# Kernel tuning notes

Measured on AMD Instinct MI355X. Metric: run time of the kernel, lower is better.

## Reference

```python
import jax, jax.numpy as jnp
import numpy as np

NUM_LAYERS = 6
KS = 5  # kernel_size; also attention window size K
EPS_IN = 1e-5  # torch InstanceNorm1d default eps


def _conv1d(x, w, b, d, p):
    # x: [N,C,L], w: [O,I,KS], dilated 'same' conv
    y = jax.lax.conv_general_dilated(x, w, window_strides=(1,), padding=[(p, p)],
                                     rhs_dilation=(d,), dimension_numbers=('NCH', 'OIH', 'NCH'))
    return y + b[None, :, None]


def _pw(x, w, b):
    # pointwise (1x1) conv: x [N,C,L], w [O,C]
    return jnp.einsum('oc,ncl->nol', w, x) + b[None, :, None]


def _layer(x, x_cross, pr, d):
    C, L = x.shape[1], x.shape[2]
    p = (KS // 2) * d  # padding
    conv_w, conv_b, qw, qb, kw, kb, vw, vb, f1w, f1b, f2w, f2b = pr
    out1 = _conv1d(x, conv_w, conv_b, d, p)
    xc = jnp.concatenate([x, x_cross], axis=1)
    q = _pw(xc, qw, qb)            # [N,C,L]
    k = _pw(xc, kw, kb)
    v = _pw(x, vw, vb)
    kp = jnp.pad(k, ((0, 0), (0, 0), (p, p)))
    vp = jnp.pad(v, ((0, 0), (0, 0), (p, p)))
    # attn index for query q, slot j is (q + j*d) into padded axis -> shifted slices
    win_k = jnp.stack([kp[:, :, j * d:j * d + L] for j in range(KS)], axis=-1)  # [N,C,L,K]
    win_v = jnp.stack([vp[:, :, j * d:j * d + L] for j in range(KS)], axis=-1)
    att = jnp.einsum('ncl,nclk->nlk', q, win_k) / np.float32(np.sqrt(C))
    pos = jnp.arange(L)[:, None] + (jnp.arange(KS)[None, :] - KS // 2) * d  # absolute key pos
    mask = (pos >= 0) & (pos < L)  # [L,K]
    att = jax.nn.softmax(att + jnp.log(mask + 1e-6), axis=-1) * mask
    r = jnp.einsum('nlk,nclk->ncl', att, win_v)
    h = out1 + r
    # InstanceNorm1d (no affine): normalize over L per (n,c)
    mu = jnp.mean(h, axis=2, keepdims=True)
    var = jnp.var(h, axis=2, keepdims=True)
    h = (h - mu) * jax.lax.rsqrt(var + EPS_IN)
    out = _pw(jax.nn.relu(_pw(h, f1w, f1b)), f2w, f2b)
    return x + out


def reference(x, x_cross, time_emb, time_w, time_b, conv_w, conv_b, qw, qb, kw, kb, vw, vb, f1w, f1b, f2w, f2b):
    te = time_emb * jax.nn.sigmoid(time_emb)  # swish
    x = x + (te @ time_w.T + time_b)[:, :, None]
    for i in range(NUM_LAYERS):
        pr = (conv_w[i], conv_b[i], qw[i], qb[i], kw[i], kb[i], vw[i], vb[i],
              f1w[i], f1b[i], f2w[i], f2b[i])
        x = _layer(x, x_cross, pr, 2 ** i)
    return x


def setup_inputs() -> dict:
    N, C, CC, L, T, nL = 4, 256, 256, 4096, 512, NUM_LAYERS
    key = jax.random.key(0)
    ks = jax.random.split(key, 18)
    s = 0.05
    return {
        'x': jax.random.normal(ks[0], (N, C, L), jnp.float32),
        'x_cross': jax.random.normal(ks[1], (N, CC, L), jnp.float32),
        'time_emb': jax.random.normal(ks[2], (N, T), jnp.float32),
        'time_w': jax.random.normal(ks[3], (C, T), jnp.float32) * s,
        'time_b': jax.random.normal(ks[4], (C,), jnp.float32) * s,
        'conv_w': jax.random.normal(ks[5], (nL, C, C, KS), jnp.float32) * s,
        'conv_b': jax.random.normal(ks[6], (nL, C), jnp.float32) * s,
        'qw': jax.random.normal(ks[7], (nL, C, C + CC), jnp.float32) * s,
        'qb': jax.random.normal(ks[8], (nL, C), jnp.float32) * s,
        'kw': jax.random.normal(ks[9], (nL, C, C + CC), jnp.float32) * s,
        'kb': jax.random.normal(ks[10], (nL, C), jnp.float32) * s,
        'vw': jax.random.normal(ks[11], (nL, C, C), jnp.float32) * s,
        'vb': jax.random.normal(ks[12], (nL, C), jnp.float32) * s,
        'f1w': jax.random.normal(ks[13], (nL, C, C), jnp.float32) * s,
        'f1b': jax.random.normal(ks[14], (nL, C), jnp.float32) * s,
        'f2w': jax.random.normal(ks[15], (nL, C, C), jnp.float32) * s,
        'f2b': jax.random.normal(ks[16], (nL, C), jnp.float32) * s,
    }
```

## Files before the change

kernel.cpp:

```cpp
#include <hip/hip_runtime.h>
#include <hip/hip_bf16.h>
#include <cstddef>
#include <cstdint>

#define N_   4
#define C_   256
#define L_   4096
#define T_   512
#define KS_  5
#define NL_  6
#define HALO 64
#define LP_  (L_ + 2 * HALO)
#define XCS  512
#define NCH  256

typedef __attribute__((ext_vector_type(8))) __bf16 bf16x8;
typedef __attribute__((ext_vector_type(4))) float f32x4;

#define VM_WAIT3 asm volatile("s_waitcnt vmcnt(3)" ::: "memory")
#define VM_WAIT0 asm volatile("s_waitcnt vmcnt(0)" ::: "memory")

__device__ __forceinline__ void gload_lds16(const void* g, void* l) {
    __builtin_amdgcn_global_load_lds(
        (const __attribute__((address_space(1))) unsigned int*)g,
        (__attribute__((address_space(3))) unsigned int*)l, 16, 0, 0);
}
__device__ __forceinline__ float bf2f(unsigned short u) {
    union { unsigned int i; float f; } x; x.i = ((unsigned int)u) << 16; return x.f;
}
__device__ __forceinline__ unsigned short f2bf(float f) {
    __hip_bfloat16 h = __float2bfloat16(f);
    return *reinterpret_cast<unsigned short*>(&h);
}
__device__ __forceinline__ float4 ld4bf(const unsigned short* p) {
    ushort4 u = *reinterpret_cast<const ushort4*>(p);
    return make_float4(bf2f(u.x), bf2f(u.y), bf2f(u.z), bf2f(u.w));
}
__device__ __forceinline__ int swz(int row, int seg) { return seg ^ ((row >> 1) & 3); }

__device__ __forceinline__ void mfma16(bf16x8 af[4], bf16x8 bfr[4], f32x4 acc[4][4])
{
    #pragma unroll
    for (int m = 0; m < 4; m++)
        #pragma unroll
        for (int nn = 0; nn < 4; nn++)
            acc[m][nn] = __builtin_amdgcn_mfma_f32_16x16x32_bf16(af[m], bfr[nn], acc[m][nn], 0, 0, 0);
}

__global__ __launch_bounds__(512) void gemm_cq(
    const unsigned short* __restrict__ xcat,
    const unsigned short* __restrict__ wqkv, const float* __restrict__ qkvbias,
    const unsigned short* __restrict__ wconv, const float* __restrict__ cbias,
    unsigned short* __restrict__ qkvb, unsigned short* __restrict__ convb, int d)
{
    __shared__ alignas(16) unsigned short As[3][256 * 32];
    __shared__ alignas(16) unsigned short Bs[3][128 * 32];
    const int tid = threadIdx.x, wid = tid >> 6, lane = tid & 63;
    const int wr = wid >> 1, wc = wid & 1;
    const int r0 = blockIdx.x * 256;
    const int n = r0 >> 12, lb = r0 & (L_ - 1);
    const int ob = blockIdx.y;
    const bool isconv = (ob < 2);
    f32x4 acc[4][4] = {};
    const int orow = (lane >> 4) * 4, ocol = lane & 15;
    const int rsel = lane & 15, j = lane >> 4;

    auto read_frags = [&](const unsigned short* A, const unsigned short* B,
                          bf16x8 af[4], bf16x8 bfr[4]) {
        #pragma unroll
        for (int m = 0; m < 4; m++) {
            const int r = wr * 64 + m * 16 + rsel;
            af[m] = *reinterpret_cast<const bf16x8*>(&A[r * 32 + swz(r, j) * 8]);
        }
        #pragma unroll
        for (int nn = 0; nn < 4; nn++) {
            const int r = wc * 64 + nn * 16 + rsel;
            bfr[nn] = *reinterpret_cast<const bf16x8*>(&B[r * 32 + swz(r, j) * 8]);
        }
    };

    if (isconv) {
        const int o0 = ob * 128;
        auto stage = [&](int t, int b) {
            const int tap = t >> 3, kb = (t & 7) * 32;
            const size_t abase = (size_t)((long)n * LP_ + HALO + lb + (tap - 2) * d) * XCS;
            const unsigned short* Wj = wconv + (size_t)tap * C_ * C_;
            #pragma unroll
            for (int i = 0; i < 2; i++) {
                const int s = tid + i * 512, row = s >> 2, seg = s & 3;
                gload_lds16(xcat + abase + (size_t)row * XCS + kb + swz(row, seg) * 8,
                            As[b] + s * 8);
            }
            {
                const int row = tid >> 2, seg = tid & 3;
                gload_lds16(Wj + (size_t)(o0 + row) * C_ + kb + swz(row, seg) * 8,
                            Bs[b] + tid * 8);
            }
        };
        const int NT = 40;
        stage(0, 0); stage(1, 1);
        VM_WAIT3;
        __builtin_amdgcn_s_barrier();
        for (int t = 0; t < NT; t++) {
            const int cur = t % 3;
            bf16x8 af[4], bfr[4];
            read_frags(As[cur], Bs[cur], af, bfr);
            if (t + 2 < NT) stage(t + 2, (t + 2) % 3);
            mfma16(af, bfr, acc);
            if (t + 2 < NT) { VM_WAIT3; } else { VM_WAIT0; }
            __builtin_amdgcn_s_barrier();
        }
        #pragma unroll
        for (int m = 0; m < 4; m++)
            #pragma unroll
            for (int nn = 0; nn < 4; nn++) {
                const int gr0 = r0 + wr * 64 + m * 16 + orow;
                const int gc = o0 + wc * 64 + nn * 16 + ocol;
                const float bv = cbias[gc];
                #pragma unroll
                for (int rr = 0; rr < 4; rr++)
                    convb[(size_t)(gr0 + rr) * C_ + gc] = f2bf(acc[m][nn][rr] + bv);
            }
    } else {
        const int o0 = (ob - 2) * 128;
        const size_t abase = ((size_t)n * LP_ + HALO + lb) * XCS;
        auto stage = [&](int t, int b) {
            const int kb = t * 32;
            #pragma unroll
            for (int i = 0; i < 2; i++) {
                const int s = tid + i * 512, row = s >> 2, seg = s & 3;
                gload_lds16(xcat + abase + (size_t)row * XCS + kb + swz(row, seg) * 8,
                            As[b] + s * 8);
            }
            {
                const int row = tid >> 2, seg = tid & 3;
                gload_lds16(wqkv + (size_t)(o0 + row) * 512 + kb + swz(row, seg) * 8,
                            Bs[b] + tid * 8);
            }
        };
        const int NT = (o0 >= 512) ? 8 : 16;
        stage(0, 0); stage(1, 1);
        VM_WAIT3;
        __builtin_amdgcn_s_barrier();
        for (int t = 0; t < NT; t++) {
            const int cur = t % 3;
            bf16x8 af[4], bfr[4];
            read_frags(As[cur], Bs[cur], af, bfr);
            if (t + 2 < NT) stage(t + 2, (t + 2) % 3);
            mfma16(af, bfr, acc);
            if (t + 2 < NT) { VM_WAIT3; } else { VM_WAIT0; }
            __builtin_amdgcn_s_barrier();
        }
        #pragma unroll
        for (int m = 0; m < 4; m++)
            #pragma unroll
            for (int nn = 0; nn < 4; nn++) {
                const int gr0 = r0 + wr * 64 + m * 16 + orow;
                const int gc = o0 + wc * 64 + nn * 16 + ocol;
                const float bv = qkvbias[gc];
                #pragma unroll
                for (int rr = 0; rr < 4; rr++)
                    qkvb[(size_t)(gr0 + rr) * 768 + gc] = f2bf(acc[m][nn][rr] + bv);
            }
    }
}

template <int EP, int PERN>
__global__ __launch_bounds__(256) void gemm_f(
    const unsigned short* __restrict__ A,
    const unsigned short* __restrict__ B,
    const float* __restrict__ bias,
    unsigned short* __restrict__ outb,
    float* __restrict__ xres, unsigned short* __restrict__ xcat)
{
    __shared__ alignas(16) unsigned short As[3][64 * 32];
    __shared__ alignas(16) unsigned short Bs[3][128 * 32];
    const int tid = threadIdx.x, wid = tid >> 6, lane = tid & 63;
    const int wr = wid >> 1, wc = wid & 1;
    const int r0 = blockIdx.x * 64;
    const int o0 = blockIdx.y * 128;
    const int n = r0 >> 12;
    if (PERN) {
        B += (size_t)n * C_ * C_;
        bias += n * C_;
    }
    const size_t abase = (size_t)r0 * C_;
    const int rsel = lane & 15, j = lane >> 4;
    f32x4 acc[2][4] = {};
    auto stage = [&](int t, int b) {
        const int kb = t * 32;
        {
            const int row = tid >> 2, seg = tid & 3;
            gload_lds16(A + abase + (size_t)row * C_ + kb + swz(row, seg) * 8, As[b] + tid * 8);
        }
        #pragma unroll
        for (int i = 0; i < 2; i++) {
            const int s = tid + i * 256, row = s >> 2, seg = s & 3;
            gload_lds16(B + (size_t)(o0 + row) * C_ + kb + swz(row, seg) * 8, Bs[b] + s * 8);
        }
    };
    const int NT = 8;
    stage(0, 0); stage(1, 1);
    VM_WAIT3;
    __builtin_amdgcn_s_barrier();
    for (int t = 0; t < NT; t++) {
        const int cur = t % 3;
        bf16x8 af[2], bfr[4];
        #pragma unroll
        for (int m = 0; m < 2; m++) {
            const int r = wr * 32 + m * 16 + rsel;
            af[m] = *reinterpret_cast<const bf16x8*>(&As[cur][r * 32 + swz(r, j) * 8]);
        }
        #pragma unroll
        for (int nn = 0; nn < 4; nn++) {
            const int r = wc * 64 + nn * 16 + rsel;
            bfr[nn] = *reinterpret_cast<const bf16x8*>(&Bs[cur][r * 32 + swz(r, j) * 8]);
        }
        if (t + 2 < NT) stage(t + 2, (t + 2) % 3);
        #pragma unroll
        for (int m = 0; m < 2; m++)
            #pragma unroll
            for (int nn = 0; nn < 4; nn++)
                acc[m][nn] = __builtin_amdgcn_mfma_f32_16x16x32_bf16(af[m], bfr[nn], acc[m][nn], 0, 0, 0);
        if (t + 2 < NT) { VM_WAIT3; } else { VM_WAIT0; }
        __builtin_amdgcn_s_barrier();
    }
    const int orow = (lane >> 4) * 4, ocol = lane & 15;
    #pragma unroll
    for (int m = 0; m < 2; m++)
        #pragma unroll
        for (int nn = 0; nn < 4; nn++) {
            const int gr0 = r0 + wr * 32 + m * 16 + orow;
            const int gc = o0 + wc * 64 + nn * 16 + ocol;
            const float bv = bias[gc];
            #pragma unroll
            for (int rr = 0; rr < 4; rr++) {
                const int gr = gr0 + rr;
                const float v = acc[m][nn][rr] + bv;
                if (EP == 2) {
                    outb[(size_t)gr * C_ + gc] = f2bf(fmaxf(v, 0.f));
                } else {
                    const float nv = v + xres[(size_t)gr * C_ + gc];
                    xres[(size_t)gr * C_ + gc] = nv;
                    const int n2 = gr >> 12, ll = gr & (L_ - 1);
                    xcat[((size_t)n2 * LP_ + HALO + ll) * XCS + gc] = f2bf(nv);
                }
            }
        }
}

__global__ __launch_bounds__(256) void attn_fused(
    const unsigned short* __restrict__ qkv, const unsigned short* __restrict__ convb,
    unsigned short* __restrict__ hb2, float* __restrict__ psum, float* __restrict__ psq, int d)
{
    __shared__ float ps[4][256], pq[4][256];
    const int n = blockIdx.y;
    const int wave = threadIdx.x >> 6;
    const int lane = threadIdx.x & 63;
    float acs[4] = {0.f, 0.f, 0.f, 0.f}, acq[4] = {0.f, 0.f, 0.f, 0.f};
    for (int lq = 0; lq < 4; lq++) {
        const int l = blockIdx.x * 16 + wave * 4 + lq;
        const float4 qv = ld4bf(qkv + ((size_t)n * L_ + l) * 768 + lane * 4);
        float att[KS_];
        #pragma unroll
        for (int j = 0; j < KS_; j++) {
            const int lp = l + (j - 2) * d;
            float s = 0.f;
            if (lp >= 0 && lp < L_) {
                const float4 kv = ld4bf(qkv + ((size_t)n * L_ + lp) * 768 + 256 + lane * 4);
                s = qv.x * kv.x + qv.y * kv.y + qv.z * kv.z + qv.w * kv.w;
            }
            #pragma unroll
            for (int off = 32; off > 0; off >>= 1) s += __shfl_xor(s, off, 64);
            att[j] = s * 0.0625f;
        }
        float logit[KS_], m = -1e30f;
        #pragma unroll
        for (int j = 0; j < KS_; j++) {
            const int lp = l + (j - 2) * d;
            logit[j] = att[j] + logf(((lp >= 0 && lp < L_) ? 1.f : 0.f) + 1e-6f);
            m = fmaxf(m, logit[j]);
        }
        float den = 0.f, wgt[KS_];
        #pragma unroll
        for (int j = 0; j < KS_; j++) { wgt[j] = expf(logit[j] - m); den += wgt[j]; }
        const float inv = 1.f / den;
        float4 r = {0.f, 0.f, 0.f, 0.f};
        #pragma unroll
        for (int j = 0; j < KS_; j++) {
            const int lp = l + (j - 2) * d;
            if (lp < 0 || lp >= L_) continue;
            const float wj = wgt[j] * inv;
            const float4 vv = ld4bf(qkv + ((size_t)n * L_ + lp) * 768 + 512 + lane * 4);
            r.x += wj * vv.x; r.y += wj * vv.y; r.z += wj * vv.z; r.w += wj * vv.w;
        }
        const size_t rowoff = ((size_t)n * L_ + l) * C_ + lane * 4;
        const float4 cv = ld4bf(convb + rowoff);
        const float h0 = cv.x + r.x, h1 = cv.y + r.y, h2 = cv.z + r.z, h3 = cv.w + r.w;
        ushort4 ho;
        ho.x = f2bf(h0); ho.y = f2bf(h1); ho.z = f2bf(h2); ho.w = f2bf(h3);
        *(ushort4*)(hb2 + rowoff) = ho;
        acs[0] += h0; acs[1] += h1; acs[2] += h2; acs[3] += h3;
        acq[0] += h0 * h0; acq[1] += h1 * h1; acq[2] += h2 * h2; acq[3] += h3 * h3;
    }
    const int cb4 = lane * 4;
    #pragma unroll
    for (int u = 0; u < 4; u++) { ps[wave][cb4 + u] = acs[u]; pq[wave][cb4 + u] = acq[u]; }
    __syncthreads();
    const int t = threadIdx.x;
    psum[((size_t)n * NCH + blockIdx.x) * C_ + t] = ps[0][t] + ps[1][t] + ps[2][t] + ps[3][t];
    psq[((size_t)n * NCH + blockIdx.x) * C_ + t] = pq[0][t] + pq[1][t] + pq[2][t] + pq[3][t];
}

__global__ __launch_bounds__(256) void norm_red(
    const float* __restrict__ psum, const float* __restrict__ psq,
    float* __restrict__ psum2, float* __restrict__ psq2)
{
    const int g = blockIdx.x, n = blockIdx.y, c = threadIdx.x;
    float s = 0.f, ss = 0.f;
    for (int ch = g * 16; ch < g * 16 + 16; ch++) {
        s += psum[((size_t)n * NCH + ch) * C_ + c];
        ss += psq[((size_t)n * NCH + ch) * C_ + c];
    }
    psum2[((size_t)n * 16 + g) * C_ + c] = s;
    psq2[((size_t)n * 16 + g) * C_ + c] = ss;
}

__global__ __launch_bounds__(256) void fold_f1(
    const float* __restrict__ f1w, const float* __restrict__ f1b,
    const float* __restrict__ psum2, const float* __restrict__ psq2,
    unsigned short* __restrict__ W1p, float* __restrict__ b1eff)
{
    const int b = blockIdx.x;
    const int n = b >> 8, o = b & 255;
    const int c = threadIdx.x;
    const int lane = c & 63, wid = c >> 6;
    float s = 0.f, ss = 0.f;
    #pragma unroll
    for (int g = 0; g < 16; g++) {
        s += psum2[((size_t)n * 16 + g) * C_ + c];
        ss += psq2[((size_t)n * 16 + g) * C_ + c];
    }
    const float mu = s * (1.f / L_);
    const float scv = rsqrtf(ss * (1.f / L_) - mu * mu + 1e-5f);
    const float w = f1w[o * C_ + c];
    W1p[((size_t)n * C_ + o) * C_ + c] = f2bf(w * scv);
    float part = w * mu * scv;
    #pragma unroll
    for (int off = 32; off > 0; off >>= 1) part += __shfl_xor(part, off, 64);
    __shared__ float red[4];
    if (lane == 0) red[wid] = part;
    __syncthreads();
    if (c == 0) b1eff[n * C_ + o] = f1b[o] - (red[0] + red[1] + red[2] + red[3]);
}

__global__ __launch_bounds__(128) void time_bias_kernel(
    const float* __restrict__ te, const float* __restrict__ tw,
    const float* __restrict__ tb, float* __restrict__ bias)
{
    int nc = blockIdx.x;
    int n = nc >> 8, c = nc & 255;
    int tid = threadIdx.x;
    float s = 0.f;
    for (int t = tid; t < T_; t += 128) {
        float e = te[n * T_ + t];
        s += (e / (1.f + expf(-e))) * tw[c * T_ + t];
    }
    __shared__ float red[128];
    red[tid] = s;
    __syncthreads();
    for (int off = 64; off > 0; off >>= 1) {
        if (tid < off) red[tid] += red[tid + off];
        __syncthreads();
    }
    if (tid == 0) bias[nc] = red[0] + tb[c];
}

__global__ __launch_bounds__(256) void halo_zero(unsigned short* __restrict__ xcat)
{
    const int t = blockIdx.x * 256 + threadIdx.x;
    const int n = t >> 14, rr = (t >> 7) & 127, c4 = t & 127;
    const int row = (rr < 64) ? rr : (L_ + HALO) + (rr - 64);
    ushort4 z = {0, 0, 0, 0};
    *(ushort4*)(xcat + ((size_t)n * LP_ + row) * XCS + c4 * 4) = z;
}

template <int MODE>
__global__ __launch_bounds__(256) void transpose_in(
    const float* __restrict__ in, const float* __restrict__ bias,
    float* __restrict__ xres, unsigned short* __restrict__ xcat)
{
    __shared__ float tile[32][33];
    const int n = blockIdx.z;
    const int l0 = blockIdx.x * 32, c0 = blockIdx.y * 32;
    const int tx = threadIdx.x, ty = threadIdx.y;
    #pragma unroll
    for (int i = 0; i < 4; i++) {
        int c = c0 + ty + 8 * i;
        tile[ty + 8 * i][tx] = in[((size_t)n * C_ + c) * L_ + l0 + tx];
    }
    __syncthreads();
    #pragma unroll
    for (int i = 0; i < 4; i++) {
        const int l = l0 + ty + 8 * i;
        const int c = c0 + tx;
        float v = tile[tx][ty + 8 * i];
        if (MODE == 0) {
            v += bias[n * C_ + c];
            xres[((size_t)n * L_ + l) * C_ + c] = v;
            xcat[((size_t)n * LP_ + HALO + l) * XCS + c] = f2bf(v);
        } else {
            xcat[((size_t)n * LP_ + HALO + l) * XCS + C_ + c] = f2bf(v);
        }
    }
}

__global__ __launch_bounds__(256) void transpose_out(
    const float* __restrict__ in, float* __restrict__ out)
{
    __shared__ float tile[32][33];
    const int n = blockIdx.z;
    const int l0 = blockIdx.x * 32, c0 = blockIdx.y * 32;
    const int tx = threadIdx.x, ty = threadIdx.y;
    #pragma unroll
    for (int i = 0; i < 4; i++) {
        int l = l0 + ty + 8 * i;
        tile[ty + 8 * i][tx] = in[((size_t)n * L_ + l) * C_ + c0 + tx];
    }
    __syncthreads();
    #pragma unroll
    for (int i = 0; i < 4; i++) {
        int c = c0 + ty + 8 * i;
        out[((size_t)n * C_ + c) * L_ + l0 + tx] = tile[tx][ty + 8 * i];
    }
}

__global__ __launch_bounds__(256) void prep_qkv(
    const float* __restrict__ qw, const float* __restrict__ kw, const float* __restrict__ vw,
    const float* __restrict__ qb, const float* __restrict__ kb, const float* __restrict__ vb,
    unsigned short* __restrict__ W, float* __restrict__ Bias)
{
    const size_t idx = (size_t)blockIdx.x * 256 + threadIdx.x;
    const int layer = (int)(idx / (768 * 512));
    const int rem = (int)(idx % (768 * 512));
    const int row = rem >> 9, k = rem & 511;
    float v;
    if (row < 256) v = qw[((size_t)layer * 256 + row) * 512 + k];
    else if (row < 512) v = kw[((size_t)layer * 256 + row - 256) * 512 + k];
    else v = (k < 256) ? vw[((size_t)layer * 256 + row - 512) * 256 + k] : 0.f;
    W[idx] = f2bf(v);
    if (k == 0) {
        float b;
        if (row < 256) b = qb[layer * 256 + row];
        else if (row < 512) b = kb[layer * 256 + row - 256];
        else b = vb[layer * 256 + row - 512];
        Bias[layer * 768 + row] = b;
    }
}

__global__ __launch_bounds__(256) void prep_conv(
    const float* __restrict__ cw, unsigned short* __restrict__ W)
{
    const size_t idx = (size_t)blockIdx.x * 256 + threadIdx.x;
    const int layer = (int)(idx / (KS_ * C_ * C_));
    const int rem = (int)(idx % (KS_ * C_ * C_));
    const int j = rem / (C_ * C_);
    const int o = (rem / C_) & 255, c = rem & 255;
    W[idx] = f2bf(cw[(((size_t)layer * C_ + o) * C_ + c) * KS_ + j]);
}

__global__ __launch_bounds__(256) void conv_f2bf(
    const float* __restrict__ in, unsigned short* __restrict__ out, int nelem)
{
    const int idx = blockIdx.x * 256 + threadIdx.x;
    if (idx < nelem) out[idx] = f2bf(in[idx]);
}

extern "C" void kernel_launch(void* const* d_in, const int* in_sizes, int n_in,
                              void* d_out, int out_size, void* d_ws, size_t ws_size,
                              hipStream_t stream)
{
    (void)in_sizes; (void)n_in; (void)out_size; (void)ws_size;
    const float* x   = (const float*)d_in[0];
    const float* xc  = (const float*)d_in[1];
    const float* te  = (const float*)d_in[2];
    const float* tw  = (const float*)d_in[3];
    const float* tb  = (const float*)d_in[4];
    const float* cw  = (const float*)d_in[5];
    const float* cb  = (const float*)d_in[6];
    const float* qw  = (const float*)d_in[7];
    const float* qbi = (const float*)d_in[8];
    const float* kw  = (const float*)d_in[9];
    const float* kbi = (const float*)d_in[10];
    const float* vw  = (const float*)d_in[11];
    const float* vbi = (const float*)d_in[12];
    const float* f1w = (const float*)d_in[13];
    const float* f1b = (const float*)d_in[14];
    const float* f2w = (const float*)d_in[15];
    const float* f2b = (const float*)d_in[16];

    char* p = (char*)d_ws;
    auto alloc = [&](size_t bytes) { char* r = p; p += (bytes + 255) & ~(size_t)255; return r; };
    const size_t NLC = (size_t)N_ * L_ * C_;
    float* xres  = (float*)alloc(NLC * 4);
    unsigned short* xcat  = (unsigned short*)alloc((size_t)N_ * LP_ * XCS * 2);
    unsigned short* qkvb  = (unsigned short*)alloc((size_t)N_ * L_ * 768 * 2);
    unsigned short* convb = (unsigned short*)alloc(NLC * 2);
    unsigned short* hb2   = (unsigned short*)alloc(NLC * 2);
    unsigned short* f1ob  = (unsigned short*)alloc(NLC * 2);
    unsigned short* wqkvb = (unsigned short*)alloc((size_t)NL_ * 768 * 512 * 2);
    unsigned short* wconvb= (unsigned short*)alloc((size_t)NL_ * KS_ * C_ * C_ * 2);
    unsigned short* wf2b  = (unsigned short*)alloc((size_t)NL_ * C_ * C_ * 2);
    unsigned short* W1p   = (unsigned short*)alloc((size_t)N_ * C_ * C_ * 2);
    float* b1eff  = (float*)alloc((size_t)N_ * C_ * 4);
    float* qkvbias = (float*)alloc((size_t)NL_ * 768 * 4);
    float* biasb = (float*)alloc(N_ * C_ * 4);
    float* psum  = (float*)alloc((size_t)N_ * NCH * C_ * 4);
    float* psq   = (float*)alloc((size_t)N_ * NCH * C_ * 4);
    float* psum2 = (float*)alloc((size_t)N_ * 16 * C_ * 4);
    float* psq2  = (float*)alloc((size_t)N_ * 16 * C_ * 4);

    halo_zero<<<256, 256, 0, stream>>>(xcat);
    prep_qkv<<<(NL_ * 768 * 512) / 256, 256, 0, stream>>>(qw, kw, vw, qbi, kbi, vbi, wqkvb, qkvbias);
    prep_conv<<<(NL_ * KS_ * C_ * C_) / 256, 256, 0, stream>>>(cw, wconvb);
    conv_f2bf<<<(NL_ * C_ * C_) / 256, 256, 0, stream>>>(f2w, wf2b, NL_ * C_ * C_);

    time_bias_kernel<<<N_ * C_, 128, 0, stream>>>(te, tw, tb, biasb);
    dim3 tgrid(L_ / 32, C_ / 32, N_), tblk(32, 8);
    transpose_in<0><<<tgrid, tblk, 0, stream>>>(x, biasb, xres, xcat);
    transpose_in<1><<<tgrid, tblk, 0, stream>>>(xc, nullptr, nullptr, xcat);

    for (int i = 0; i < NL_; i++) {
        const int d = 1 << i;
        gemm_cq<<<dim3(64, 8), 512, 0, stream>>>(
            xcat, wqkvb + (size_t)i * 768 * 512, qkvbias + i * 768,
            wconvb + (size_t)i * KS_ * C_ * C_, cb + i * C_, qkvb, convb, d);
        attn_fused<<<dim3(L_ / 16, N_), 256, 0, stream>>>(qkvb, convb, hb2, psum, psq, d);
        norm_red<<<dim3(16, N_), 256, 0, stream>>>(psum, psq, psum2, psq2);
        fold_f1<<<N_ * C_, 256, 0, stream>>>(
            f1w + (size_t)i * C_ * C_, f1b + i * C_, psum2, psq2, W1p, b1eff);
        gemm_f<2, 1><<<dim3(256, 2), 256, 0, stream>>>(
            hb2, W1p, b1eff, f1ob, nullptr, nullptr);
        gemm_f<3, 0><<<dim3(256, 2), 256, 0, stream>>>(
            f1ob, wf2b + (size_t)i * C_ * C_, f2b + i * C_, nullptr, xres, xcat);
    }
    transpose_out<<<tgrid, tblk, 0, stream>>>(xres, (float*)d_out);
}
```

Before: 496.8 us.

## Drop fp32 residual stream, keep residual in bf16 xcat; shrink gemm_f tiles

```diff
diff --git a/kernel.cpp b/kernel.cpp
--- a/kernel.cpp
+++ b/kernel.cpp
@@ -18,6 +18,7 @@
 typedef __attribute__((ext_vector_type(4))) float f32x4;
 
 #define VM_WAIT3 asm volatile("s_waitcnt vmcnt(3)" ::: "memory")
+#define VM_WAIT2 asm volatile("s_waitcnt vmcnt(2)" ::: "memory")
 #define VM_WAIT0 asm volatile("s_waitcnt vmcnt(0)" ::: "memory")
 
 __device__ __forceinline__ void gload_lds16(const void* g, void* l) {
@@ -171,14 +172,13 @@
     const unsigned short* __restrict__ B,
     const float* __restrict__ bias,
     unsigned short* __restrict__ outb,
-    float* __restrict__ xres, unsigned short* __restrict__ xcat)
+    unsigned short* __restrict__ xcat)
 {
     __shared__ alignas(16) unsigned short As[3][64 * 32];
-    __shared__ alignas(16) unsigned short Bs[3][128 * 32];
+    __shared__ alignas(16) unsigned short Bs[3][64 * 32];
     const int tid = threadIdx.x, wid = tid >> 6, lane = tid & 63;
-    const int wr = wid >> 1, wc = wid & 1;
     const int r0 = blockIdx.x * 64;
-    const int o0 = blockIdx.y * 128;
+    const int o0 = blockIdx.y * 64;
     const int n = r0 >> 12;
     if (PERN) {
         B += (size_t)n * C_ * C_;
@@ -186,67 +186,56 @@
     }
     const size_t abase = (size_t)r0 * C_;
     const int rsel = lane & 15, j = lane >> 4;
-    f32x4 acc[2][4] = {};
+    f32x4 acc[4] = {};
     auto stage = [&](int t, int b) {
         const int kb = t * 32;
-        {
-            const int row = tid >> 2, seg = tid & 3;
-            gload_lds16(A + abase + (size_t)row * C_ + kb + swz(row, seg) * 8, As[b] + tid * 8);
-        }
-        #pragma unroll
-        for (int i = 0; i < 2; i++) {
-            const int s = tid + i * 256, row = s >> 2, seg = s & 3;
-            gload_lds16(B + (size_t)(o0 + row) * C_ + kb + swz(row, seg) * 8, Bs[b] + s * 8);
-        }
+        const int row = tid >> 2, seg = tid & 3;
+        const int gso = swz(row, seg) * 8;
+        gload_lds16(A + abase + (size_t)row * C_ + kb + gso, As[b] + tid * 8);
+        gload_lds16(B + (size_t)(o0 + row) * C_ + kb + gso, Bs[b] + tid * 8);
     };
     const int NT = 8;
     stage(0, 0); stage(1, 1);
-    VM_WAIT3;
+    VM_WAIT2;
     __builtin_amdgcn_s_barrier();
     for (int t = 0; t < NT; t++) {
         const int cur = t % 3;
-        bf16x8 af[2], bfr[4];
-        #pragma unroll
-        for (int m = 0; m < 2; m++) {
-            const int r = wr * 32 + m * 16 + rsel;
-            af[m] = *reinterpret_cast<const bf16x8*>(&As[cur][r * 32 + swz(r, j) * 8]);
+        bf16x8 af, bfr[4];
+        {
+            const int r = wid * 16 + rsel;
+            af = *reinterpret_cast<const bf16x8*>(&As[cur][r * 32 + swz(r, j) * 8]);
         }
         #pragma unroll
         for (int nn = 0; nn < 4; nn++) {
-            const int r = wc * 64 + nn * 16 + rsel;
+            const int r = nn * 16 + rsel;
             bfr[nn] = *reinterpret_cast<const bf16x8*>(&Bs[cur][r * 32 + swz(r, j) * 8]);
         }
         if (t + 2 < NT) stage(t + 2, (t + 2) % 3);
         #pragma unroll
-        for (int m = 0; m < 2; m++)
-            #pragma unroll
-            for (int nn = 0; nn < 4; nn++)
-                acc[m][nn] = __builtin_amdgcn_mfma_f32_16x16x32_bf16(af[m], bfr[nn], acc[m][nn], 0, 0, 0);
-        if (t + 2 < NT) { VM_WAIT3; } else { VM_WAIT0; }
+        for (int nn = 0; nn < 4; nn++)
+            acc[nn] = __builtin_amdgcn_mfma_f32_16x16x32_bf16(af, bfr[nn], acc[nn], 0, 0, 0);
+        if (t + 2 < NT) { VM_WAIT2; } else { VM_WAIT0; }
         __builtin_amdgcn_s_barrier();
     }
     const int orow = (lane >> 4) * 4, ocol = lane & 15;
     #pragma unroll
-    for (int m = 0; m < 2; m++)
-        #pragma unroll
-        for (int nn = 0; nn < 4; nn++) {
-            const int gr0 = r0 + wr * 32 + m * 16 + orow;
-            const int gc = o0 + wc * 64 + nn * 16 + ocol;
-            const float bv = bias[gc];
-            #pragma unroll
-            for (int rr = 0; rr < 4; rr++) {
-                const int gr = gr0 + rr;
-                const float v = acc[m][nn][rr] + bv;
-                if (EP == 2) {
-                    outb[(size_t)gr * C_ + gc] = f2bf(fmaxf(v, 0.f));
-                } else {
-                    const float nv = v + xres[(size_t)gr * C_ + gc];
-                    xres[(size_t)gr * C_ + gc] = nv;
-                    const int n2 = gr >> 12, ll = gr & (L_ - 1);
-                    xcat[((size_t)n2 * LP_ + HALO + ll) * XCS + gc] = f2bf(nv);
-                }
-            }
-        }
+    for (int nn = 0; nn < 4; nn++) {
+        const int gr0 = r0 + wid * 16 + orow;
+        const int gc = o0 + nn * 16 + ocol;
+        const float bv = bias[gc];
+        #pragma unroll
+        for (int rr = 0; rr < 4; rr++) {
+            const int gr = gr0 + rr;
+            const float v = acc[nn][rr] + bv;
+            if (EP == 2) {
+                outb[(size_t)gr * C_ + gc] = f2bf(fmaxf(v, 0.f));
+            } else {
+                const int n2 = gr >> 12, ll = gr & (L_ - 1);
+                unsigned short* xp = xcat + ((size_t)n2 * LP_ + HALO + ll) * XCS + gc;
+                *xp = f2bf(v + bf2f(*xp));
+            }
+        }
+    }
 }
 
 __global__ __launch_bounds__(256) void attn_fused(
@@ -388,7 +377,7 @@
 template <int MODE>
 __global__ __launch_bounds__(256) void transpose_in(
     const float* __restrict__ in, const float* __restrict__ bias,
-    float* __restrict__ xres, unsigned short* __restrict__ xcat)
+    unsigned short* __restrict__ xcat)
 {
     __shared__ float tile[32][33];
     const int n = blockIdx.z;
@@ -407,7 +396,6 @@
         float v = tile[tx][ty + 8 * i];
         if (MODE == 0) {
             v += bias[n * C_ + c];
-            xres[((size_t)n * L_ + l) * C_ + c] = v;
             xcat[((size_t)n * LP_ + HALO + l) * XCS + c] = f2bf(v);
         } else {
             xcat[((size_t)n * LP_ + HALO + l) * XCS + C_ + c] = f2bf(v);
@@ -416,7 +404,7 @@
 }
 
 __global__ __launch_bounds__(256) void transpose_out(
-    const float* __restrict__ in, float* __restrict__ out)
+    const unsigned short* __restrict__ xcat, float* __restrict__ out)
 {
     __shared__ float tile[32][33];
     const int n = blockIdx.z;
@@ -425,7 +413,7 @@
     #pragma unroll
     for (int i = 0; i < 4; i++) {
         int l = l0 + ty + 8 * i;
-        tile[ty + 8 * i][tx] = in[((size_t)n * L_ + l) * C_ + c0 + tx];
+        tile[ty + 8 * i][tx] = bf2f(xcat[((size_t)n * LP_ + HALO + l) * XCS + c0 + tx]);
     }
     __syncthreads();
     #pragma unroll
@@ -502,7 +490,6 @@
     char* p = (char*)d_ws;
     auto alloc = [&](size_t bytes) { char* r = p; p += (bytes + 255) & ~(size_t)255; return r; };
     const size_t NLC = (size_t)N_ * L_ * C_;
-    float* xres  = (float*)alloc(NLC * 4);
     unsigned short* xcat  = (unsigned short*)alloc((size_t)N_ * LP_ * XCS * 2);
     unsigned short* qkvb  = (unsigned short*)alloc((size_t)N_ * L_ * 768 * 2);
     unsigned short* convb = (unsigned short*)alloc(NLC * 2);
@@ -527,8 +514,8 @@
 
     time_bias_kernel<<<N_ * C_, 128, 0, stream>>>(te, tw, tb, biasb);
     dim3 tgrid(L_ / 32, C_ / 32, N_), tblk(32, 8);
-    transpose_in<0><<<tgrid, tblk, 0, stream>>>(x, biasb, xres, xcat);
-    transpose_in<1><<<tgrid, tblk, 0, stream>>>(xc, nullptr, nullptr, xcat);
+    transpose_in<0><<<tgrid, tblk, 0, stream>>>(x, biasb, xcat);
+    transpose_in<1><<<tgrid, tblk, 0, stream>>>(xc, nullptr, xcat);
 
     for (int i = 0; i < NL_; i++) {
         const int d = 1 << i;
@@ -539,10 +526,10 @@
         norm_red<<<dim3(16, N_), 256, 0, stream>>>(psum, psq, psum2, psq2);
         fold_f1<<<N_ * C_, 256, 0, stream>>>(
             f1w + (size_t)i * C_ * C_, f1b + i * C_, psum2, psq2, W1p, b1eff);
-        gemm_f<2, 1><<<dim3(256, 2), 256, 0, stream>>>(
-            hb2, W1p, b1eff, f1ob, nullptr, nullptr);
-        gemm_f<3, 0><<<dim3(256, 2), 256, 0, stream>>>(
-            f1ob, wf2b + (size_t)i * C_ * C_, f2b + i * C_, nullptr, xres, xcat);
-    }
-    transpose_out<<<tgrid, tblk, 0, stream>>>(xres, (float*)d_out);
-}
+        gemm_f<2, 1><<<dim3(256, 4), 256, 0, stream>>>(
+            hb2, W1p, b1eff, f1ob, nullptr);
+        gemm_f<3, 0><<<dim3(256, 4), 256, 0, stream>>>(
+            f1ob, wf2b + (size_t)i * C_ * C_, f2b + i * C_, nullptr, xcat);
+    }
+    transpose_out<<<tgrid, tblk, 0, stream>>>(xcat, (float*)d_out);
+}
```

Result: faster. 476.3 us (-4.1%).
